# Kernel tuning notes

Hardware: AMD Instinct MI355X
Metric: run time of the kernel (lower is better)

Reference implementation:

```python
import jax, jax.numpy as jnp
import numpy as np

NEG_SLOPE = 0.2
EPS = 1e-16  # matches PyG-style segment softmax denominator guard

N_NODES = 50000
N_EDGES = 800000
IN_CH = 256
HEADS = 4
OUT_CH = 32


def setup_inputs() -> dict:
    key = jax.random.key(0)
    k1, k2, k3, k4 = jax.random.split(key, 4)
    nodes_ft = jax.random.normal(k1, (N_NODES, IN_CH), dtype=jnp.float32)
    adj_list = jax.random.randint(k2, (2, N_EDGES), 0, N_NODES, dtype=jnp.int64)
    # xavier-normal-ish scales
    weight = jax.random.normal(k3, (IN_CH, HEADS * OUT_CH), dtype=jnp.float32) * (
        (2.0 / (IN_CH + HEADS * OUT_CH)) ** 0.5
    )
    att = jax.random.normal(k4, (1, HEADS, 2 * OUT_CH), dtype=jnp.float32) * (
        (2.0 / (1 + 2 * OUT_CH)) ** 0.5
    )
    bias = jnp.zeros((HEADS * OUT_CH,), dtype=jnp.float32)
    return {"nodes_ft": nodes_ft, "adj_list": adj_list, "weight": weight, "att": att, "bias": bias}


def reference(nodes_ft, adj_list, weight, att, bias):
    N = nodes_ft.shape[0]
    H, C = att.shape[1], att.shape[2] // 2
    dst = adj_list[0]  # softmax / aggregation key
    src = adj_list[1]
    # node hidden states: [N, H, C]
    h = (nodes_ft @ weight).reshape(N, H, C)
    xi = h[dst]  # [E, H, C]
    xj = h[src]  # [E, H, C]
    # attention logits: cat([xi, xj]) . att  ==  xi.att_i + xj.att_j
    att_i, att_j = att[:, :, :C], att[:, :, C:]
    alpha = (xi * att_i).sum(-1) + (xj * att_j).sum(-1)  # [E, H]
    alpha = jax.nn.leaky_relu(alpha, negative_slope=NEG_SLOPE)
    # segment softmax over destination node
    m = jax.ops.segment_max(alpha, dst, num_segments=N)  # [N, H]
    m = jnp.where(jnp.isfinite(m), m, 0.0)
    e = jnp.exp(alpha - m[dst])
    s = jax.ops.segment_sum(e, dst, num_segments=N)  # [N, H]
    a = e / (s[dst] + EPS)  # [E, H]
    # weighted scatter-add aggregate
    vals = xj * a[:, :, None]  # [E, H, C]
    out = jax.ops.segment_sum(vals, dst, num_segments=N)  # [N, H, C]
    out = out.reshape(N, H * C) + bias  # concat=True
    return out
```

## Files before the change

kernel.cpp:

```cpp
#include <hip/hip_runtime.h>
#include <math.h>

#define NN 50000
#define NE 800000
#define IN_CH 256
#define HEADS 4
#define OUT_CH 32
#define HC 128
#define NEG_SLOPE 0.2f
#define GAT_EPS 1e-16f

#define SBS 1024
#define NB  ((NN + SBS - 1) / SBS)

#define OFF_H      0
#define OFF_AI     (NN*HC)
#define OFF_AJ     (OFF_AI + NN*HEADS)
#define OFF_ROW    (OFF_AJ + NN*HEADS)
#define OFF_CUR    (OFF_ROW + NN + 4)
#define OFF_HIST   (OFF_CUR + NN + 4)
#define OFF_BSUM   (OFF_HIST + NN + 4)
#define OFF_BOFF   (OFF_BSUM + NB + 4)
#define OFF_ESRC   (OFF_BOFF + NB + 4)

__global__ void k_zero(int* __restrict__ hist) {
    int i = blockIdx.x * blockDim.x + threadIdx.x;
    if (i < NN) hist[i] = 0;
}

#define BM 64
#define BK 32
__global__ __launch_bounds__(256) void k_gemm(const float* __restrict__ A,
                                              const float* __restrict__ W,
                                              float* __restrict__ H) {
    __shared__ float sA[BM][BK + 4];
    __shared__ float sW[BK][HC];
    const int tid = threadIdx.x;
    const int row0 = blockIdx.x * BM;
    const int c0 = (tid & 15) * 8;
    const int r0 = (tid >> 4) * 4;

    float acc[4][8];
#pragma unroll
    for (int i = 0; i < 4; i++)
#pragma unroll
        for (int j = 0; j < 8; j++) acc[i][j] = 0.0f;

    for (int k0 = 0; k0 < IN_CH; k0 += BK) {
#pragma unroll
        for (int l = 0; l < 2; l++) {
            int f4 = tid + l * 256;
            int r = f4 >> 3;
            int kk = (f4 & 7) * 4;
            int grow = row0 + r;
            float4 v = make_float4(0.f, 0.f, 0.f, 0.f);
            if (grow < NN) v = *(const float4*)&A[(size_t)grow * IN_CH + k0 + kk];
            *(float4*)&sA[r][kk] = v;
        }
#pragma unroll
        for (int l = 0; l < 4; l++) {
            int f4 = tid + l * 256;
            int r = f4 >> 5;
            int cc = (f4 & 31) * 4;
            *(float4*)&sW[r][cc] = *(const float4*)&W[(size_t)(k0 + r) * HC + cc];
        }
        __syncthreads();
#pragma unroll
        for (int k = 0; k < BK; k++) {
            float av[4];
#pragma unroll
            for (int i = 0; i < 4; i++) av[i] = sA[r0 + i][k];
            float wv[8];
            *(float4*)&wv[0] = *(float4*)&sW[k][c0];
            *(float4*)&wv[4] = *(float4*)&sW[k][c0 + 4];
#pragma unroll
            for (int i = 0; i < 4; i++)
#pragma unroll
                for (int j = 0; j < 8; j++)
                    acc[i][j] = fmaf(av[i], wv[j], acc[i][j]);
        }
        __syncthreads();
    }
#pragma unroll
    for (int i = 0; i < 4; i++) {
        int grow = row0 + r0 + i;
        if (grow < NN) {
            float4 o0 = make_float4(acc[i][0], acc[i][1], acc[i][2], acc[i][3]);
            float4 o1 = make_float4(acc[i][4], acc[i][5], acc[i][6], acc[i][7]);
            *(float4*)&H[(size_t)grow * HC + c0] = o0;
            *(float4*)&H[(size_t)grow * HC + c0 + 4] = o1;
        }
    }
}

__global__ void k_att(const float* __restrict__ Hm, const float* __restrict__ att,
                      float* __restrict__ ai, float* __restrict__ aj) {
    int idx = blockIdx.x * blockDim.x + threadIdx.x;
    if (idx >= NN * HEADS) return;
    int n = idx >> 2, hh = idx & 3;
    const float* hp  = Hm + (size_t)n * HC + hh * OUT_CH;
    const float* ati = att + hh * 2 * OUT_CH;
    const float* atj = ati + OUT_CH;
    float si = 0.f, sj = 0.f;
#pragma unroll
    for (int c = 0; c < OUT_CH; c++) {
        float hv = hp[c];
        si = fmaf(hv, ati[c], si);
        sj = fmaf(hv, atj[c], sj);
    }
    ai[idx] = si;
    aj[idx] = sj;
}

__global__ void k_hist(const int* __restrict__ adj, int* __restrict__ hist) {
    int e = blockIdx.x * blockDim.x + threadIdx.x;
    if (e < NE) atomicAdd(&hist[adj[e]], 1);
}

__global__ __launch_bounds__(256) void k_bsum(const int* __restrict__ hist,
                                              int* __restrict__ bsum) {
    int b = blockIdx.x, t = threadIdx.x;
    int i0 = b * SBS + t * 4;
    int s = 0;
#pragma unroll
    for (int j = 0; j < 4; j++) {
        int i = i0 + j;
        if (i < NN) s += hist[i];
    }
#pragma unroll
    for (int off = 32; off; off >>= 1) s += __shfl_xor(s, off);
    __shared__ int ws[4];
    int lane = t & 63, wid = t >> 6;
    if (lane == 0) ws[wid] = s;
    __syncthreads();
    if (t == 0) bsum[b] = ws[0] + ws[1] + ws[2] + ws[3];
}

__global__ __launch_bounds__(64) void k_bscan(const int* __restrict__ bsum,
                                              int* __restrict__ boff) {
    int lane = threadIdx.x;
    int v = (lane < NB) ? bsum[lane] : 0;
    int inc = v;
#pragma unroll
    for (int off = 1; off < 64; off <<= 1) {
        int u = __shfl_up(inc, off);
        if (lane >= off) inc += u;
    }
    if (lane < NB) boff[lane] = inc - v;
}

__global__ __launch_bounds__(256) void k_bwrite(const int* __restrict__ hist,
                                                const int* __restrict__ boff,
                                                int* __restrict__ row,
                                                int* __restrict__ cur) {
    int b = blockIdx.x, t = threadIdx.x;
    int i0 = b * SBS + t * 4;
    int v[4];
    int s = 0;
#pragma unroll
    for (int j = 0; j < 4; j++) {
        int i = i0 + j;
        v[j] = (i < NN) ? hist[i] : 0;
        s += v[j];
    }
    int lane = t & 63, wid = t >> 6;
    int inc = s;
#pragma unroll
    for (int off = 1; off < 64; off <<= 1) {
        int u = __shfl_up(inc, off);
        if (lane >= off) inc += u;
    }
    __shared__ int wsum[4];
    if (lane == 63) wsum[wid] = inc;
    __syncthreads();
    int woff = 0;
    for (int w = 0; w < wid; w++) woff += wsum[w];
    int run = boff[b] + woff + (inc - s);
#pragma unroll
    for (int j = 0; j < 4; j++) {
        int i = i0 + j;
        if (i < NN) {
            row[i] = run;
            cur[i] = run;
            run += v[j];
        }
    }
    if (b == 0 && t == 0) row[NN] = NE;
}

__global__ void k_scatter(const int* __restrict__ adj, int* __restrict__ cur,
                          int* __restrict__ esrc) {
    int e = blockIdx.x * blockDim.x + threadIdx.x;
    if (e >= NE) return;
    int dst = adj[e];
    int src = adj[NE + e];
    int pos = atomicAdd(&cur[dst], 1);
    esrc[pos] = src;
}

__device__ __forceinline__ float lrelu(float x) {
    return x > 0.f ? x : NEG_SLOPE * x;
}

__global__ __launch_bounds__(256) void k_gather(const int* __restrict__ row,
                                                const int* __restrict__ esrc,
                                                const float* __restrict__ ai,
                                                const float* __restrict__ aj,
                                                const float* __restrict__ Hm,
                                                const float* __restrict__ bias,
                                                float* __restrict__ out) {
    int gid = blockIdx.x * blockDim.x + threadIdx.x;
    int nid = gid >> 6;
    int lane = gid & 63;
    if (nid >= NN) return;
    int r0 = row[nid];
    int deg = row[nid + 1] - r0;

    float4 aiv = *(const float4*)&ai[nid * 4];

    float mx0 = -INFINITY, mx1 = -INFINITY, mx2 = -INFINITY, mx3 = -INFINITY;
    for (int k = lane; k < deg; k += 64) {
        int s = esrc[r0 + k];
        float4 ajv = *(const float4*)&aj[s * 4];
        mx0 = fmaxf(mx0, lrelu(aiv.x + ajv.x));
        mx1 = fmaxf(mx1, lrelu(aiv.y + ajv.y));
        mx2 = fmaxf(mx2, lrelu(aiv.z + ajv.z));
        mx3 = fmaxf(mx3, lrelu(aiv.w + ajv.w));
    }
#pragma unroll
    for (int off = 32; off; off >>= 1) {
        mx0 = fmaxf(mx0, __shfl_xor(mx0, off));
        mx1 = fmaxf(mx1, __shfl_xor(mx1, off));
        mx2 = fmaxf(mx2, __shfl_xor(mx2, off));
        mx3 = fmaxf(mx3, __shfl_xor(mx3, off));
    }

    float s0 = 0.f, s1 = 0.f, s2 = 0.f, s3 = 0.f;
    for (int k = lane; k < deg; k += 64) {
        int s = esrc[r0 + k];
        float4 ajv = *(const float4*)&aj[s * 4];
        s0 += __expf(lrelu(aiv.x + ajv.x) - mx0);
        s1 += __expf(lrelu(aiv.y + ajv.y) - mx1);
        s2 += __expf(lrelu(aiv.z + ajv.z) - mx2);
        s3 += __expf(lrelu(aiv.w + ajv.w) - mx3);
    }
#pragma unroll
    for (int off = 32; off; off >>= 1) {
        s0 += __shfl_xor(s0, off);
        s1 += __shfl_xor(s1, off);
        s2 += __shfl_xor(s2, off);
        s3 += __shfl_xor(s3, off);
    }

    int c0 = lane * 2;
    int hh = lane >> 4;
    float mh  = (hh & 2) ? ((hh & 1) ? mx3 : mx2) : ((hh & 1) ? mx1 : mx0);
    float sh  = (hh & 2) ? ((hh & 1) ? s3 : s2) : ((hh & 1) ? s1 : s0);
    float aih = (hh & 2) ? ((hh & 1) ? aiv.w : aiv.z) : ((hh & 1) ? aiv.y : aiv.x);
    float inv = 1.0f / (sh + GAT_EPS);

    float accx = 0.f, accy = 0.f;
#pragma unroll 4
    for (int k = 0; k < deg; k++) {
        int s = esrc[r0 + k];
        float al = lrelu(aih + aj[s * 4 + hh]);
        float a = __expf(al - mh) * inv;
        float2 hv = *(const float2*)&Hm[(size_t)s * HC + c0];
        accx = fmaf(hv.x, a, accx);
        accy = fmaf(hv.y, a, accy);
    }
    out[(size_t)nid * HC + c0]     = accx + bias[c0];
    out[(size_t)nid * HC + c0 + 1] = accy + bias[c0 + 1];
}

extern "C" void kernel_launch(void* const* d_in, const int* in_sizes, int n_in,
                              void* d_out, int out_size, void* d_ws, size_t ws_size,
                              hipStream_t stream) {
    const float* nodes  = (const float*)d_in[0];
    const int*   adj    = (const int*)d_in[1];
    const float* weight = (const float*)d_in[2];
    const float* att    = (const float*)d_in[3];
    const float* bias   = (const float*)d_in[4];
    float* out = (float*)d_out;
    float* ws  = (float*)d_ws;

    float* Hm   = ws + OFF_H;
    float* ai   = ws + OFF_AI;
    float* aj   = ws + OFF_AJ;
    int*   rowp = (int*)(ws + OFF_ROW);
    int*   cur  = (int*)(ws + OFF_CUR);
    int*   hist = (int*)(ws + OFF_HIST);
    int*   bsum = (int*)(ws + OFF_BSUM);
    int*   boff = (int*)(ws + OFF_BOFF);
    int*   esrc = (int*)(ws + OFF_ESRC);

    k_zero<<<(NN + 255) / 256, 256, 0, stream>>>(hist);
    k_hist<<<(NE + 255) / 256, 256, 0, stream>>>(adj, hist);
    k_bsum<<<NB, 256, 0, stream>>>(hist, bsum);
    k_bscan<<<1, 64, 0, stream>>>(bsum, boff);
    k_bwrite<<<NB, 256, 0, stream>>>(hist, boff, rowp, cur);
    k_scatter<<<(NE + 255) / 256, 256, 0, stream>>>(adj, cur, esrc);
    k_gemm<<<(NN + BM - 1) / BM, 256, 0, stream>>>(nodes, weight, Hm);
    k_att<<<(NN * HEADS + 255) / 256, 256, 0, stream>>>(Hm, att, ai, aj);
    k_gather<<<(NN * 64 + 255) / 256, 256, 0, stream>>>(rowp, esrc, ai, aj, Hm, bias, out);
}
```

Measured before the change: 316.4 us.

## Use bf16 MFMA GEMM and store hidden states in bf16 for gather

Replaces the fp32 shared-memory GEMM with a bf16 MFMA kernel that converts inputs on the fly and reads a pre-transposed bf16 weight copy. The hidden-state matrix is now stored in bf16, halving the bytes fetched per edge in the gather and the bytes read by the attention-logit kernel. It adds a small weight-transpose kernel and lowers numerical precision of H and of the attention logits.

Measured after the change: 296.7 us. -6.2%, faster.

```diff
diff --git a/kernel.cpp b/kernel.cpp
--- a/kernel.cpp
+++ b/kernel.cpp
@@ -1,4 +1,5 @@
 #include <hip/hip_runtime.h>
+#include <hip/hip_bf16.h>
 #include <math.h>
 
 #define NN 50000
@@ -13,8 +14,9 @@
 #define SBS 1024
 #define NB  ((NN + SBS - 1) / SBS)
 
-#define OFF_H      0
-#define OFF_AI     (NN*HC)
+#define OFF_HB     0
+#define OFF_WT     (NN*HC/2)
+#define OFF_AI     (OFF_WT + 16384)
 #define OFF_AJ     (OFF_AI + NN*HEADS)
 #define OFF_ROW    (OFF_AJ + NN*HEADS)
 #define OFF_CUR    (OFF_ROW + NN + 4)
@@ -23,90 +25,111 @@
 #define OFF_BOFF   (OFF_BSUM + NB + 4)
 #define OFF_ESRC   (OFF_BOFF + NB + 4)
 
+typedef __attribute__((ext_vector_type(8))) short short8v;
+typedef __attribute__((ext_vector_type(4))) float float4v;
+
+__device__ __forceinline__ unsigned short f2bf(float x) {
+    union { float f; unsigned u; } v; v.f = x;
+    unsigned r = v.u + 0x7fffu + ((v.u >> 16) & 1u);
+    return (unsigned short)(r >> 16);
+}
+__device__ __forceinline__ float bf2f(unsigned short b) {
+    union { unsigned u; float f; } v; v.u = ((unsigned)b) << 16;
+    return v.f;
+}
+
 __global__ void k_zero(int* __restrict__ hist) {
     int i = blockIdx.x * blockDim.x + threadIdx.x;
     if (i < NN) hist[i] = 0;
 }
 
-#define BM 64
-#define BK 32
+__global__ void k_wt(const float* __restrict__ W, unsigned short* __restrict__ Wt) {
+    int idx = blockIdx.x * blockDim.x + threadIdx.x;
+    if (idx >= HC * IN_CH) return;
+    int n = idx >> 8, k = idx & 255;
+    Wt[n * IN_CH + k] = f2bf(W[(size_t)k * HC + n]);
+}
+
 __global__ __launch_bounds__(256) void k_gemm(const float* __restrict__ A,
-                                              const float* __restrict__ W,
-                                              float* __restrict__ H) {
-    __shared__ float sA[BM][BK + 4];
-    __shared__ float sW[BK][HC];
-    const int tid = threadIdx.x;
-    const int row0 = blockIdx.x * BM;
-    const int c0 = (tid & 15) * 8;
-    const int r0 = (tid >> 4) * 4;
-
-    float acc[4][8];
+                                              const unsigned short* __restrict__ Wt,
+                                              unsigned short* __restrict__ Hb) {
+    const int tid  = threadIdx.x;
+    const int lane = tid & 63;
+    const int w    = tid >> 6;
+    const int wr   = w >> 1, wc = w & 1;
+    const int blockRow = blockIdx.x * 128;
+
+    const int lrow = lane & 15;
+    const int kgrp = lane >> 4;
+
+    float4v acc[4][4];
 #pragma unroll
     for (int i = 0; i < 4; i++)
 #pragma unroll
-        for (int j = 0; j < 8; j++) acc[i][j] = 0.0f;
-
-    for (int k0 = 0; k0 < IN_CH; k0 += BK) {
-#pragma unroll
-        for (int l = 0; l < 2; l++) {
-            int f4 = tid + l * 256;
-            int r = f4 >> 3;
-            int kk = (f4 & 7) * 4;
-            int grow = row0 + r;
-            float4 v = make_float4(0.f, 0.f, 0.f, 0.f);
-            if (grow < NN) v = *(const float4*)&A[(size_t)grow * IN_CH + k0 + kk];
-            *(float4*)&sA[r][kk] = v;
+        for (int j = 0; j < 4; j++) acc[i][j] = (float4v){0.f, 0.f, 0.f, 0.f};
+
+#pragma unroll
+    for (int ks = 0; ks < 8; ks++) {
+        const int kb = ks * 32 + kgrp * 8;
+        short8v af[4], bfr[4];
+#pragma unroll
+        for (int mi = 0; mi < 4; mi++) {
+            int r = blockRow + wr * 64 + mi * 16 + lrow;
+            if (r >= NN) r = NN - 1;
+            const float* ap = A + (size_t)r * IN_CH + kb;
+            float4 a0 = *(const float4*)ap;
+            float4 a1 = *(const float4*)(ap + 4);
+            short8v t;
+            t[0] = (short)f2bf(a0.x); t[1] = (short)f2bf(a0.y);
+            t[2] = (short)f2bf(a0.z); t[3] = (short)f2bf(a0.w);
+            t[4] = (short)f2bf(a1.x); t[5] = (short)f2bf(a1.y);
+            t[6] = (short)f2bf(a1.z); t[7] = (short)f2bf(a1.w);
+            af[mi] = t;
         }
 #pragma unroll
-        for (int l = 0; l < 4; l++) {
-            int f4 = tid + l * 256;
-            int r = f4 >> 5;
-            int cc = (f4 & 31) * 4;
-            *(float4*)&sW[r][cc] = *(const float4*)&W[(size_t)(k0 + r) * HC + cc];
+        for (int ni = 0; ni < 4; ni++) {
+            int c = wc * 64 + ni * 16 + lrow;
+            bfr[ni] = *(const short8v*)(Wt + (size_t)c * IN_CH + kb);
         }
-        __syncthreads();
-#pragma unroll
-        for (int k = 0; k < BK; k++) {
-            float av[4];
-#pragma unroll
-            for (int i = 0; i < 4; i++) av[i] = sA[r0 + i][k];
-            float wv[8];
-            *(float4*)&wv[0] = *(float4*)&sW[k][c0];
-            *(float4*)&wv[4] = *(float4*)&sW[k][c0 + 4];
-#pragma unroll
-            for (int i = 0; i < 4; i++)
-#pragma unroll
-                for (int j = 0; j < 8; j++)
-                    acc[i][j] = fmaf(av[i], wv[j], acc[i][j]);
+#pragma unroll
+        for (int mi = 0; mi < 4; mi++)
+#pragma unroll
+            for (int ni = 0; ni < 4; ni++)
+                acc[mi][ni] = __builtin_amdgcn_mfma_f32_16x16x32_bf16(
+                    af[mi], bfr[ni], acc[mi][ni], 0, 0, 0);
+    }
+
+#pragma unroll
+    for (int mi = 0; mi < 4; mi++) {
+#pragma unroll
+        for (int reg = 0; reg < 4; reg++) {
+            int r = blockRow + wr * 64 + mi * 16 + kgrp * 4 + reg;
+            if (r >= NN) continue;
+#pragma unroll
+            for (int ni = 0; ni < 4; ni++) {
+                int c = wc * 64 + ni * 16 + lrow;
+                Hb[(size_t)r * HC + c] = f2bf(acc[mi][ni][reg]);
+            }
         }
-        __syncthreads();
-    }
-#pragma unroll
-    for (int i = 0; i < 4; i++) {
-        int grow = row0 + r0 + i;
-        if (grow < NN) {
-            float4 o0 = make_float4(acc[i][0], acc[i][1], acc[i][2], acc[i][3]);
-            float4 o1 = make_float4(acc[i][4], acc[i][5], acc[i][6], acc[i][7]);
-            *(float4*)&H[(size_t)grow * HC + c0] = o0;
-            *(float4*)&H[(size_t)grow * HC + c0 + 4] = o1;
-        }
-    }
-}
-
-__global__ void k_att(const float* __restrict__ Hm, const float* __restrict__ att,
+    }
+}
+
+__global__ void k_att(const unsigned short* __restrict__ Hb, const float* __restrict__ att,
                       float* __restrict__ ai, float* __restrict__ aj) {
     int idx = blockIdx.x * blockDim.x + threadIdx.x;
     if (idx >= NN * HEADS) return;
     int n = idx >> 2, hh = idx & 3;
-    const float* hp  = Hm + (size_t)n * HC + hh * OUT_CH;
+    const unsigned* hp = (const unsigned*)(Hb + (size_t)n * HC + hh * OUT_CH);
     const float* ati = att + hh * 2 * OUT_CH;
     const float* atj = ati + OUT_CH;
     float si = 0.f, sj = 0.f;
 #pragma unroll
-    for (int c = 0; c < OUT_CH; c++) {
-        float hv = hp[c];
-        si = fmaf(hv, ati[c], si);
-        sj = fmaf(hv, atj[c], sj);
+    for (int i = 0; i < 16; i++) {
+        unsigned u = hp[i];
+        float lo = bf2f((unsigned short)(u & 0xffff));
+        float hi = bf2f((unsigned short)(u >> 16));
+        si = fmaf(lo, ati[2 * i], si);     si = fmaf(hi, ati[2 * i + 1], si);
+        sj = fmaf(lo, atj[2 * i], sj);     sj = fmaf(hi, atj[2 * i + 1], sj);
     }
     ai[idx] = si;
     aj[idx] = sj;
@@ -174,7 +197,7 @@
     if (lane == 63) wsum[wid] = inc;
     __syncthreads();
     int woff = 0;
-    for (int w = 0; w < wid; w++) woff += wsum[w];
+    for (int w2 = 0; w2 < wid; w2++) woff += wsum[w2];
     int run = boff[b] + woff + (inc - s);
 #pragma unroll
     for (int j = 0; j < 4; j++) {
@@ -206,7 +229,7 @@
                                                 const int* __restrict__ esrc,
                                                 const float* __restrict__ ai,
                                                 const float* __restrict__ aj,
-                                                const float* __restrict__ Hm,
+                                                const unsigned short* __restrict__ Hb,
                                                 const float* __restrict__ bias,
                                                 float* __restrict__ out) {
     int gid = blockIdx.x * blockDim.x + threadIdx.x;
@@ -265,9 +288,9 @@
         int s = esrc[r0 + k];
         float al = lrelu(aih + aj[s * 4 + hh]);
         float a = __expf(al - mh) * inv;
-        float2 hv = *(const float2*)&Hm[(size_t)s * HC + c0];
-        accx = fmaf(hv.x, a, accx);
-        accy = fmaf(hv.y, a, accy);
+        unsigned hu = *(const unsigned*)(Hb + (size_t)s * HC + c0);
+        accx = fmaf(bf2f((unsigned short)(hu & 0xffff)), a, accx);
+        accy = fmaf(bf2f((unsigned short)(hu >> 16)), a, accy);
     }
     out[(size_t)nid * HC + c0]     = accx + bias[c0];
     out[(size_t)nid * HC + c0 + 1] = accy + bias[c0 + 1];
@@ -284,7 +307,8 @@
     float* out = (float*)d_out;
     float* ws  = (float*)d_ws;
 
-    float* Hm   = ws + OFF_H;
+    unsigned short* Hb = (unsigned short*)(ws + OFF_HB);
+    unsigned short* Wt = (unsigned short*)(ws + OFF_WT);
     float* ai   = ws + OFF_AI;
     float* aj   = ws + OFF_AJ;
     int*   rowp = (int*)(ws + OFF_ROW);
@@ -300,7 +324,8 @@
     k_bscan<<<1, 64, 0, stream>>>(bsum, boff);
     k_bwrite<<<NB, 256, 0, stream>>>(hist, boff, rowp, cur);
     k_scatter<<<(NE + 255) / 256, 256, 0, stream>>>(adj, cur, esrc);
-    k_gemm<<<(NN + BM - 1) / BM, 256, 0, stream>>>(nodes, weight, Hm);
-    k_att<<<(NN * HEADS + 255) / 256, 256, 0, stream>>>(Hm, att, ai, aj);
-    k_gather<<<(NN * 64 + 255) / 256, 256, 0, stream>>>(rowp, esrc, ai, aj, Hm, bias, out);
-}
+    k_wt<<<(HC * IN_CH + 255) / 256, 256, 0, stream>>>(weight, Wt);
+    k_gemm<<<(NN + 127) / 128, 256, 0, stream>>>(nodes, Wt, Hb);
+    k_att<<<(NN * HEADS + 255) / 256, 256, 0, stream>>>(Hb, att, ai, aj);
+    k_gather<<<(NN * 64 + 255) / 256, 256, 0, stream>>>(rowp, esrc, ai, aj, Hb, bias, out);
+}
```
